# Kernel tuning notes

Measured on AMD Instinct MI355X. Metric: run time of the kernel, lower is better.

Reference implementation:

```python
import jax, jax.numpy as jnp
import numpy as np

DIM = 512
NUM_GROUPS = 32
NUM_HEADS = 8
EPS = 1e-5


def group_norm(x, gamma, beta):
    # x: (B, C, H, W); normalize over (C//G, H, W) per group
    B, C, H, W = x.shape
    g = x.reshape(B, NUM_GROUPS, -1)
    mean = g.mean(axis=2, keepdims=True)
    var = g.var(axis=2, keepdims=True)
    g = (g - mean) * jax.lax.rsqrt(var + EPS)
    x = g.reshape(B, C, H, W)
    return x * gamma[None, :, None, None] + beta[None, :, None, None]


def setup_inputs() -> dict:
    key = jax.random.key(0)
    ks = jax.random.split(key, 7)
    B, C, H, W = 16, DIM, 32, 32
    x = jax.random.normal(ks[0], (B, C, H, W), dtype=jnp.float32)
    gamma = jnp.ones((C,), dtype=jnp.float32)
    beta = jnp.zeros((C,), dtype=jnp.float32)
    s_in = 1.0 / np.sqrt(C)
    w_qkv = jax.random.normal(ks[1], (3 * C, C), dtype=jnp.float32) * s_in
    b_qkv = jnp.zeros((3 * C,), dtype=jnp.float32)
    w_proj = jax.random.normal(ks[2], (C, C), dtype=jnp.float32) * s_in
    b_proj = jnp.zeros((C,), dtype=jnp.float32)
    return {"x": x, "gamma": gamma, "beta": beta, "w_qkv": w_qkv,
            "b_qkv": b_qkv, "w_proj": w_proj, "b_proj": b_proj}


def reference(x, gamma, beta, w_qkv, b_qkv, w_proj, b_proj):
    B, C, H, W = x.shape
    nh = NUM_HEADS
    c3 = 3 * C // nh          # per-head qkv channels (3 * head_dim)
    dh = C // nh              # head_dim
    scale = C ** (-0.5)       # NOTE: source scales by full dim, not head_dim

    h = group_norm(x, gamma, beta)

    # 1x1 conv qkv projection: (B, 3C, H, W)
    qkv = jnp.einsum('bchw,oc->bohw', h, w_qkv) + b_qkv[None, :, None, None]

    # rearrange 'b (head c) h w -> (b head) (h w) c'
    qkv = qkv.reshape(B, nh, c3, H, W)
    qkv = qkv.transpose(0, 1, 3, 4, 2).reshape(B * nh, H * W, c3)
    q, k, v = jnp.split(qkv, 3, axis=2)   # each (B*nh, HW, dh)

    score = jnp.einsum('bnc,bmc->bnm', q, k * scale)   # (B*nh, HW, HW)
    attn = jax.nn.softmax(score, axis=2)
    out = jnp.einsum('bnm,bmc->bnc', attn, v)          # (B*nh, HW, dh)

    # rearrange '(head b) (h w) c -> b (head c) h w'  (NOTE head-major, as in source)
    out = out.reshape(nh, B, H, W, dh)
    out = out.transpose(1, 0, 4, 2, 3).reshape(B, C, H, W)

    out = jnp.einsum('bchw,oc->bohw', out, w_proj) + b_proj[None, :, None, None]
    return out + x
```

## Files before the change

kernel.cpp:

```cpp
#include <hip/hip_runtime.h>
#include <stdint.h>

typedef __bf16 bf16;
typedef __attribute__((ext_vector_type(4))) float f32x4;
typedef __attribute__((ext_vector_type(16))) float f32x16;
typedef __attribute__((ext_vector_type(4))) int i32x4;
typedef __attribute__((ext_vector_type(8))) __bf16 bf16x8;
typedef __attribute__((ext_vector_type(4))) __bf16 bf16x4;

#define NB 16
#define CH 512
#define HWS 1024
#define NHEAD 8
#define DH 64
#define O3 1536
#define CPQ 136
#define CPF 132
#define OPD 72

__device__ __forceinline__ void gload_lds16(const bf16* g, bf16* l) {
    __builtin_amdgcn_global_load_lds(
        (const __attribute__((address_space(1))) unsigned int*)g,
        (__attribute__((address_space(3))) unsigned int*)l,
        16, 0, 0);
}

#if defined(__has_builtin) && __has_builtin(__builtin_amdgcn_exp2f)
__device__ __forceinline__ float fast_exp2(float x) { return __builtin_amdgcn_exp2f(x); }
#else
__device__ __forceinline__ float fast_exp2(float x) { return exp2f(x); }
#endif

__device__ __forceinline__ unsigned int pkbf(float a, float b) {
    unsigned short lo = __builtin_bit_cast(unsigned short, (bf16)a);
    unsigned short hi = __builtin_bit_cast(unsigned short, (bf16)b);
    return (unsigned int)lo | ((unsigned int)hi << 16);
}

__global__ void prep(const float* __restrict__ x, float* __restrict__ stats,
                     const float* __restrict__ wq, const float* __restrict__ wp,
                     bf16* __restrict__ wq_b, bf16* __restrict__ wp_b) {
    int bx = blockIdx.x;
    if (bx < 512) {
        int b = bx >> 5, g = bx & 31;
        const float4* p = (const float4*)(x + ((size_t)(b * CH + g * 16)) * HWS);
        float s = 0.f, ss = 0.f;
        for (int i = threadIdx.x; i < 4096; i += 256) {
            float4 v = p[i];
            s  += v.x + v.y + v.z + v.w;
            ss += v.x*v.x + v.y*v.y + v.z*v.z + v.w*v.w;
        }
        for (int off = 32; off; off >>= 1) {
            s  += __shfl_xor(s,  off, 64);
            ss += __shfl_xor(ss, off, 64);
        }
        __shared__ float red[8];
        int w = threadIdx.x >> 6;
        if ((threadIdx.x & 63) == 0) { red[w*2] = s; red[w*2+1] = ss; }
        __syncthreads();
        if (threadIdx.x == 0) {
            float S  = red[0] + red[2] + red[4] + red[6];
            float SS = red[1] + red[3] + red[5] + red[7];
            float mean = S * (1.f/16384.f);
            float var  = SS * (1.f/16384.f) - mean*mean;
            stats[bx*2]   = mean;
            stats[bx*2+1] = rsqrtf(var + 1e-5f);
        }
    } else {
        int i = (bx - 512) * 256 + threadIdx.x;
        if (i < O3*CH) wq_b[i] = (bf16)wq[i];
        else           wp_b[i - O3*CH] = (bf16)wp[i - O3*CH];
    }
}

__global__ void gn_apply_t(const float* __restrict__ x, const float* __restrict__ stats,
                           const float* __restrict__ gamma, const float* __restrict__ beta,
                           bf16* __restrict__ hT) {
    __shared__ float tile[32][33];
    int bx = blockIdx.x;
    int b = bx >> 9;
    int rem = bx & 511;
    int ct = rem >> 5, nt = rem & 31;
    int tx = threadIdx.x & 31, ty = threadIdx.x >> 5;
    #pragma unroll
    for (int r = 0; r < 4; ++r) {
        int c = ct*32 + ty + r*8;
        int n = nt*32 + tx;
        float v = x[((size_t)(b * CH + c)) * HWS + n];
        int g = c >> 4;
        float mean = stats[(b*32+g)*2], rstd = stats[(b*32+g)*2+1];
        tile[ty + r*8][tx] = (v - mean) * rstd * gamma[c] + beta[c];
    }
    __syncthreads();
    #pragma unroll
    for (int r = 0; r < 4; ++r) {
        int n = nt*32 + ty + r*8;
        int c = ct*32 + tx;
        hT[((size_t)(b * HWS + n)) * CH + c] = (bf16)tile[tx][ty + r*8];
    }
}

__global__ __launch_bounds__(256, 3)
void qkv_gemm(const bf16* __restrict__ W, const bf16* __restrict__ hT,
              const float* __restrict__ bias, bf16* __restrict__ qkv,
              bf16* __restrict__ vT) {
    __shared__ __align__(16) bf16 SMEM[128*CPQ];
    bf16* As = SMEM;
    bf16* Bs = SMEM + 8192;
    int bx = blockIdx.x;
    int po = bx >> 7, qo = bx & 127;
    int obase = po*128, bnbase = qo*128;
    int tid = threadIdx.x;
    int lane = tid & 63, w = tid >> 6;
    int quad = lane >> 4, l15 = lane & 15;
    int wm = w >> 1, wn = w & 1;
    int x7 = l15 & 7;
    int srow = lane >> 3, spos = lane & 7;
    int sgc = (spos ^ srow) * 8;

    f32x4 acc[4][4] = {};
    for (int k0 = 0; k0 < 512; k0 += 64) {
        #pragma unroll
        for (int r = 0; r < 4; ++r) {
            int rb = r*32 + w*8;
            gload_lds16(W  + ((size_t)(obase  + rb + srow))*512 + k0 + sgc, &As[rb*64]);
            gload_lds16(hT + ((size_t)(bnbase + rb + srow))*512 + k0 + sgc, &Bs[rb*64]);
        }
        __syncthreads();
        #pragma unroll
        for (int ks = 0; ks < 2; ++ks) {
            int ch = (ks*4 + quad) ^ x7;
            bf16x8 af[4], bfv[4];
            #pragma unroll
            for (int mt = 0; mt < 4; ++mt)
                af[mt] = *(const bf16x8*)(&As[(wm*64 + mt*16 + l15)*64 + ch*8]);
            #pragma unroll
            for (int nt = 0; nt < 4; ++nt)
                bfv[nt] = *(const bf16x8*)(&Bs[(wn*64 + nt*16 + l15)*64 + ch*8]);
            #pragma unroll
            for (int mt = 0; mt < 4; ++mt)
                #pragma unroll
                for (int nt = 0; nt < 4; ++nt)
                    acc[mt][nt] = __builtin_amdgcn_mfma_f32_16x16x32_bf16(af[mt], bfv[nt], acc[mt][nt], 0, 0, 0);
        }
        __syncthreads();
    }

    bf16* Cs = SMEM;
    int b = bnbase >> 10;
    int nbase = bnbase & 1023;
    #pragma unroll
    for (int mt = 0; mt < 4; ++mt) {
        int o0 = obase + wm*64 + mt*16 + quad*4;
        float4 bb = *(const float4*)(bias + o0);
        int c192 = o0 % 192;
        bool isV = (c192 >= 128);
        int h = o0 / 192;
        int d0 = c192 - 128;
        #pragma unroll
        for (int nt = 0; nt < 4; ++nt) {
            int bn_l = wn*64 + nt*16 + l15;
            bf16x4 v;
            v[0] = (bf16)(acc[mt][nt][0] + bb.x);
            v[1] = (bf16)(acc[mt][nt][1] + bb.y);
            v[2] = (bf16)(acc[mt][nt][2] + bb.z);
            v[3] = (bf16)(acc[mt][nt][3] + bb.w);
            *(bf16x4*)(&Cs[bn_l*CPQ + (o0 - obase)]) = v;
            if (isV) {
                int key = nbase + bn_l;
                size_t vb_ = ((size_t)((b*8 + h)*64 + d0)) * HWS + key;
                vT[vb_]          = v[0];
                vT[vb_ + HWS]    = v[1];
                vT[vb_ + 2*HWS]  = v[2];
                vT[vb_ + 3*HWS]  = v[3];
            }
        }
    }
    __syncthreads();
    #pragma unroll
    for (int p = 0; p < 8; ++p) {
        int bn_l = p*16 + (tid >> 4);
        int o8 = (tid & 15) * 8;
        if ((obase + o8) % 192 < 128) {
            uint4 v = *(const uint4*)(&Cs[bn_l*CPQ + o8]);
            *(uint4*)(qkv + ((size_t)(bnbase + bn_l)) * O3 + obase + o8) = v;
        }
    }
}

__global__ __launch_bounds__(256, 3)
void flash_attn(const bf16* __restrict__ qkv, const bf16* __restrict__ vT,
                bf16* __restrict__ A2) {
    __shared__ __align__(16) bf16 Ks[2][64*64];
    __shared__ __align__(16) bf16 Vs[2][64*64];
    __shared__ __align__(16) bf16 Ps[4][32*OPD];
    int bx = blockIdx.x;
    int g = bx & 127, qt = bx >> 7;
    int b = g >> 3, h = g & 7;
    int tid = threadIdx.x, lane = tid & 63, w = tid >> 6;
    int l31 = lane & 31, hi = lane >> 5;
    bool hib = (hi != 0);
    int x7l = l31 & 7;
    int srow = lane >> 3, spos = lane & 7;
    int sgc = (spos ^ srow) * 8;
    const float kLog2 = 0.04419417382415922f * 1.44269504088896341f;

    bf16x8 aq[4];
    {
        int qrow = qt*128 + w*32 + l31;
        const bf16* qb = qkv + ((size_t)(b * HWS + qrow)) * O3 + h*192 + hi*8;
        #pragma unroll
        for (int seg = 0; seg < 4; ++seg) {
            aq[seg] = *(const bf16x8*)(qb + seg*16);
            #pragma unroll
            for (int j = 0; j < 8; ++j)
                aq[seg][j] = (bf16)((float)aq[seg][j] * kLog2);
        }
    }

    const bf16* kg = qkv + ((size_t)(b*HWS + w*16 + srow))*O3 + h*192 + 64 + sgc;
    const bf16* vg = vT  + ((size_t)(g*DH  + w*16 + srow))*HWS + sgc;

    gload_lds16(kg,                  &Ks[0][(w*16)*64]);
    gload_lds16(kg + (size_t)8*O3,   &Ks[0][(w*16 + 8)*64]);
    gload_lds16(vg,                  &Vs[0][(w*16)*64]);
    gload_lds16(vg + (size_t)8*HWS,  &Vs[0][(w*16 + 8)*64]);

    f32x16 acc[2] = {};
    f32x4 L4 = {};
    __syncthreads();

    for (int kt = 0; kt < 16; ++kt) {
        int cur = kt & 1;
        if (kt < 15) {
            gload_lds16(kg + (size_t)((kt+1)*64)*O3,     &Ks[cur^1][(w*16)*64]);
            gload_lds16(kg + (size_t)((kt+1)*64 + 8)*O3, &Ks[cur^1][(w*16 + 8)*64]);
            gload_lds16(vg + (kt+1)*64,                  &Vs[cur^1][(w*16)*64]);
            gload_lds16(vg + (size_t)8*HWS + (kt+1)*64,  &Vs[cur^1][(w*16 + 8)*64]);
        }
        const bf16* Kc = &Ks[cur][0];
        const bf16* Vc = &Vs[cur][0];

        bf16x8 pa[4];
        #pragma unroll
        for (int kb = 0; kb < 2; ++kb) {
            f32x16 z = {};
            #pragma unroll
            for (int seg = 0; seg < 4; ++seg) {
                bf16x8 ak = *(const bf16x8*)(&Kc[(kb*32 + l31)*64 + (((seg*2 + hi) ^ x7l)*8)]);
                z = __builtin_amdgcn_mfma_f32_32x32x16_bf16(ak, aq[seg], z, 0, 0, 0);
            }
            float e[16];
            #pragma unroll
            for (int r = 0; r < 16; ++r) {
                e[r] = fast_exp2(z[r]);
                L4[r & 3] += e[r];
            }
            unsigned int w8[8];
            #pragma unroll
            for (int i = 0; i < 8; ++i)
                w8[i] = pkbf(e[2*i], e[2*i + 1]);
            unsigned int p0 = __shfl_xor((int)w8[0], 32, 64);
            unsigned int p1 = __shfl_xor((int)w8[1], 32, 64);
            unsigned int p2 = __shfl_xor((int)w8[2], 32, 64);
            unsigned int p3 = __shfl_xor((int)w8[3], 32, 64);
            unsigned int p4 = __shfl_xor((int)w8[4], 32, 64);
            unsigned int p5 = __shfl_xor((int)w8[5], 32, 64);
            unsigned int p6 = __shfl_xor((int)w8[6], 32, 64);
            unsigned int p7 = __shfl_xor((int)w8[7], 32, 64);
            i32x4 f0, f1;
            f0[0] = (int)(hib ? p2 : w8[0]);
            f0[1] = (int)(hib ? p3 : w8[1]);
            f0[2] = (int)(hib ? w8[2] : p0);
            f0[3] = (int)(hib ? w8[3] : p1);
            f1[0] = (int)(hib ? p6 : w8[4]);
            f1[1] = (int)(hib ? p7 : w8[5]);
            f1[2] = (int)(hib ? w8[6] : p4);
            f1[3] = (int)(hib ? w8[7] : p5);
            pa[kb*2 + 0] = __builtin_bit_cast(bf16x8, f0);
            pa[kb*2 + 1] = __builtin_bit_cast(bf16x8, f1);
        }

        #pragma unroll
        for (int db = 0; db < 2; ++db)
            #pragma unroll
            for (int ks = 0; ks < 4; ++ks) {
                bf16x8 av = *(const bf16x8*)(&Vc[(db*32 + l31)*64 + (((ks*2 + hi) ^ x7l)*8)]);
                acc[db] = __builtin_amdgcn_mfma_f32_32x32x16_bf16(av, pa[ks], acc[db], 0, 0, 0);
            }
        __syncthreads();
    }

    float Lf = (L4[0] + L4[1]) + (L4[2] + L4[3]);
    Lf += __shfl_xor(Lf, 32, 64);
    float Linv = 1.f / Lf;

    bf16* Psw = &Ps[w][0];
    #pragma unroll
    for (int db = 0; db < 2; ++db)
        #pragma unroll
        for (int i = 0; i < 8; ++i) {
            int d = db*32 + (i >> 1)*8 + (i & 1)*2 + 4*hi;
            unsigned int wv = pkbf(acc[db][2*i] * Linv, acc[db][2*i + 1] * Linv);
            *(unsigned int*)(&Psw[l31*OPD + d]) = wv;
        }

    int bp = g & 15;
    int hp = g >> 4;
    #pragma unroll
    for (int cc = 0; cc < 4; ++cc) {
        int idx = cc*64 + lane;
        int q = idx >> 3, dcc = idx & 7;
        uint4 v = *(const uint4*)(&Psw[q*OPD + dcc*8]);
        size_t oidx = ((size_t)(bp * HWS + qt*128 + w*32 + q)) * CH + hp*64 + dcc*8;
        *(uint4*)(A2 + oidx) = v;
    }
}

__global__ __launch_bounds__(256, 3)
void proj_gemm(const bf16* __restrict__ A2, const bf16* __restrict__ Wp,
               const float* __restrict__ bias, const float* __restrict__ x,
               float* __restrict__ out) {
    __shared__ __align__(16) bf16 SMEM[16896];
    bf16* As = SMEM;
    bf16* Bs = SMEM + 8192;
    int bx = blockIdx.x;
    int po = bx >> 7, qo = bx & 127;
    int obase = po*128, bnbase = qo*128;
    int tid = threadIdx.x;
    int lane = tid & 63, w = tid >> 6;
    int quad = lane >> 4, l15 = lane & 15;
    int wm = w >> 1, wn = w & 1;
    int x7 = l15 & 7;
    int srow = lane >> 3, spos = lane & 7;
    int sgc = (spos ^ srow) * 8;

    f32x4 acc[4][4] = {};
    for (int k0 = 0; k0 < 512; k0 += 64) {
        #pragma unroll
        for (int r = 0; r < 4; ++r) {
            int rb = r*32 + w*8;
            gload_lds16(A2 + ((size_t)(bnbase + rb + srow))*512 + k0 + sgc, &As[rb*64]);
            gload_lds16(Wp + ((size_t)(obase  + rb + srow))*512 + k0 + sgc, &Bs[rb*64]);
        }
        __syncthreads();
        #pragma unroll
        for (int ks = 0; ks < 2; ++ks) {
            int ch = (ks*4 + quad) ^ x7;
            bf16x8 af[4], bfv[4];
            #pragma unroll
            for (int mt = 0; mt < 4; ++mt)
                af[mt] = *(const bf16x8*)(&As[(wm*64 + mt*16 + l15)*64 + ch*8]);
            #pragma unroll
            for (int nt = 0; nt < 4; ++nt)
                bfv[nt] = *(const bf16x8*)(&Bs[(wn*64 + nt*16 + l15)*64 + ch*8]);
            #pragma unroll
            for (int mt = 0; mt < 4; ++mt)
                #pragma unroll
                for (int nt = 0; nt < 4; ++nt)
                    acc[mt][nt] = __builtin_amdgcn_mfma_f32_16x16x32_bf16(af[mt], bfv[nt], acc[mt][nt], 0, 0, 0);
        }
        __syncthreads();
    }

    float* Cf = (float*)SMEM;
    int bb = bnbase >> 10;
    int nbase = bnbase & 1023;
    #pragma unroll
    for (int hh = 0; hh < 2; ++hh) {
        if (wm == hh) {
            #pragma unroll
            for (int mt = 0; mt < 4; ++mt)
                #pragma unroll
                for (int nt = 0; nt < 4; ++nt)
                    #pragma unroll
                    for (int r = 0; r < 4; ++r)
                        Cf[(mt*16 + quad*4 + r)*CPF + wn*64 + nt*16 + l15] = acc[mt][nt][r];
        }
        __syncthreads();
        #pragma unroll
        for (int p = 0; p < 4; ++p) {
            int ol = p*32 + (tid >> 3);
            int nl0 = (tid & 7) * 8;
            int o = obase + ol;
            float bv = bias[o];
            #pragma unroll
            for (int jj = 0; jj < 2; ++jj) {
                int nl = nl0 + jj*4;
                size_t idx = ((size_t)(bb * CH + o)) * HWS + nbase + hh*64 + nl;
                float4 xr = *(const float4*)(x + idx);
                float4 res;
                res.x = Cf[(nl+0)*CPF + ol] + bv + xr.x;
                res.y = Cf[(nl+1)*CPF + ol] + bv + xr.y;
                res.z = Cf[(nl+2)*CPF + ol] + bv + xr.z;
                res.w = Cf[(nl+3)*CPF + ol] + bv + xr.w;
                *(float4*)(out + idx) = res;
            }
        }
        __syncthreads();
    }
}

extern "C" void kernel_launch(void* const* d_in, const int* in_sizes, int n_in,
                              void* d_out, int out_size, void* d_ws, size_t ws_size,
                              hipStream_t stream) {
    const float* x      = (const float*)d_in[0];
    const float* gamma  = (const float*)d_in[1];
    const float* beta   = (const float*)d_in[2];
    const float* w_qkv  = (const float*)d_in[3];
    const float* b_qkv  = (const float*)d_in[4];
    const float* w_proj = (const float*)d_in[5];
    const float* b_proj = (const float*)d_in[6];
    float* out = (float*)d_out;

    char* ws = (char*)d_ws;
    float* stats = (float*)(ws + 0);
    bf16*  wq_b  = (bf16*)(ws + 4096);
    bf16*  wp_b  = (bf16*)(ws + 1576960);
    bf16*  hT    = (bf16*)(ws + 2101248);
    bf16*  qkv   = (bf16*)(ws + 18878464);
    bf16*  vT    = (bf16*)(ws + 69210112);
    bf16*  A2    = hT;

    prep       <<<4608, 256, 0, stream>>>(x, stats, w_qkv, w_proj, wq_b, wp_b);
    gn_apply_t <<<8192, 256, 0, stream>>>(x, stats, gamma, beta, hT);
    qkv_gemm   <<<1536, 256, 0, stream>>>(wq_b, hT, b_qkv, qkv, vT);
    flash_attn <<<1024, 256, 0, stream>>>(qkv, vT, A2);
    proj_gemm  <<<512,  256, 0, stream>>>(A2, wp_b, b_proj, x, out);
}
```

Before: 220.6 us.

## Widen flash attention blocks to 8 waves and use permlane32 swaps

The flash attention kernel now runs 512 threads per block, covering 256 query rows instead of 128, and the grid is halved. Each double-buffered K/V tile is shared by twice as many waves, which halves global K/V traffic per query, and each wave now issues one async LDS load per tensor per tile instead of two. The P-fragment exchange between half-waves now uses inline-asm v_permlane32_swap instead of eight cross-lane shuffles plus selects. The larger block and the tighter launch bound of 512 threads with 4 blocks may raise register pressure or cause spills, and there are fewer blocks to balance across compute units.

New measurement: 198.4 us. -10.1%, faster.

```diff
diff --git a/kernel.cpp b/kernel.cpp
--- a/kernel.cpp
+++ b/kernel.cpp
@@ -188,18 +188,17 @@
     }
 }
 
-__global__ __launch_bounds__(256, 3)
+__global__ __launch_bounds__(512, 4)
 void flash_attn(const bf16* __restrict__ qkv, const bf16* __restrict__ vT,
                 bf16* __restrict__ A2) {
     __shared__ __align__(16) bf16 Ks[2][64*64];
     __shared__ __align__(16) bf16 Vs[2][64*64];
-    __shared__ __align__(16) bf16 Ps[4][32*OPD];
+    __shared__ __align__(16) bf16 Ps[8][32*OPD];
     int bx = blockIdx.x;
     int g = bx & 127, qt = bx >> 7;
     int b = g >> 3, h = g & 7;
     int tid = threadIdx.x, lane = tid & 63, w = tid >> 6;
     int l31 = lane & 31, hi = lane >> 5;
-    bool hib = (hi != 0);
     int x7l = l31 & 7;
     int srow = lane >> 3, spos = lane & 7;
     int sgc = (spos ^ srow) * 8;
@@ -207,7 +206,7 @@
 
     bf16x8 aq[4];
     {
-        int qrow = qt*128 + w*32 + l31;
+        int qrow = qt*256 + w*32 + l31;
         const bf16* qb = qkv + ((size_t)(b * HWS + qrow)) * O3 + h*192 + hi*8;
         #pragma unroll
         for (int seg = 0; seg < 4; ++seg) {
@@ -218,13 +217,11 @@
         }
     }
 
-    const bf16* kg = qkv + ((size_t)(b*HWS + w*16 + srow))*O3 + h*192 + 64 + sgc;
-    const bf16* vg = vT  + ((size_t)(g*DH  + w*16 + srow))*HWS + sgc;
-
-    gload_lds16(kg,                  &Ks[0][(w*16)*64]);
-    gload_lds16(kg + (size_t)8*O3,   &Ks[0][(w*16 + 8)*64]);
-    gload_lds16(vg,                  &Vs[0][(w*16)*64]);
-    gload_lds16(vg + (size_t)8*HWS,  &Vs[0][(w*16 + 8)*64]);
+    const bf16* kg = qkv + ((size_t)(b*HWS + w*8 + srow))*O3 + h*192 + 64 + sgc;
+    const bf16* vg = vT  + ((size_t)(g*DH  + w*8 + srow))*HWS + sgc;
+
+    gload_lds16(kg, &Ks[0][w*512]);
+    gload_lds16(vg, &Vs[0][w*512]);
 
     f32x16 acc[2] = {};
     f32x4 L4 = {};
@@ -233,10 +230,8 @@
     for (int kt = 0; kt < 16; ++kt) {
         int cur = kt & 1;
         if (kt < 15) {
-            gload_lds16(kg + (size_t)((kt+1)*64)*O3,     &Ks[cur^1][(w*16)*64]);
-            gload_lds16(kg + (size_t)((kt+1)*64 + 8)*O3, &Ks[cur^1][(w*16 + 8)*64]);
-            gload_lds16(vg + (kt+1)*64,                  &Vs[cur^1][(w*16)*64]);
-            gload_lds16(vg + (size_t)8*HWS + (kt+1)*64,  &Vs[cur^1][(w*16 + 8)*64]);
+            gload_lds16(kg + (size_t)((kt+1)*64)*O3, &Ks[cur^1][w*512]);
+            gload_lds16(vg + (kt+1)*64,              &Vs[cur^1][w*512]);
         }
         const bf16* Kc = &Ks[cur][0];
         const bf16* Vc = &Vs[cur][0];
@@ -260,25 +255,16 @@
             #pragma unroll
             for (int i = 0; i < 8; ++i)
                 w8[i] = pkbf(e[2*i], e[2*i + 1]);
-            unsigned int p0 = __shfl_xor((int)w8[0], 32, 64);
-            unsigned int p1 = __shfl_xor((int)w8[1], 32, 64);
-            unsigned int p2 = __shfl_xor((int)w8[2], 32, 64);
-            unsigned int p3 = __shfl_xor((int)w8[3], 32, 64);
-            unsigned int p4 = __shfl_xor((int)w8[4], 32, 64);
-            unsigned int p5 = __shfl_xor((int)w8[5], 32, 64);
-            unsigned int p6 = __shfl_xor((int)w8[6], 32, 64);
-            unsigned int p7 = __shfl_xor((int)w8[7], 32, 64);
-            i32x4 f0, f1;
-            f0[0] = (int)(hib ? p2 : w8[0]);
-            f0[1] = (int)(hib ? p3 : w8[1]);
-            f0[2] = (int)(hib ? w8[2] : p0);
-            f0[3] = (int)(hib ? w8[3] : p1);
-            f1[0] = (int)(hib ? p6 : w8[4]);
-            f1[1] = (int)(hib ? p7 : w8[5]);
-            f1[2] = (int)(hib ? w8[6] : p4);
-            f1[3] = (int)(hib ? w8[7] : p5);
-            pa[kb*2 + 0] = __builtin_bit_cast(bf16x8, f0);
-            pa[kb*2 + 1] = __builtin_bit_cast(bf16x8, f1);
+            #pragma unroll
+            for (int kl = 0; kl < 2; ++kl) {
+                unsigned int a0 = w8[4*kl + 0], a1 = w8[4*kl + 1];
+                unsigned int b0 = w8[4*kl + 2], b1 = w8[4*kl + 3];
+                asm("v_permlane32_swap_b32 %0, %1" : "+v"(a0), "+v"(b0));
+                asm("v_permlane32_swap_b32 %0, %1" : "+v"(a1), "+v"(b1));
+                i32x4 f;
+                f[0] = (int)a0; f[1] = (int)a1; f[2] = (int)b0; f[3] = (int)b1;
+                pa[kb*2 + kl] = __builtin_bit_cast(bf16x8, f);
+            }
         }
 
         #pragma unroll
@@ -312,7 +298,7 @@
         int idx = cc*64 + lane;
         int q = idx >> 3, dcc = idx & 7;
         uint4 v = *(const uint4*)(&Psw[q*OPD + dcc*8]);
-        size_t oidx = ((size_t)(bp * HWS + qt*128 + w*32 + q)) * CH + hp*64 + dcc*8;
+        size_t oidx = ((size_t)(bp * HWS + qt*256 + w*32 + q)) * CH + hp*64 + dcc*8;
         *(uint4*)(A2 + oidx) = v;
     }
 }
@@ -425,6 +411,6 @@
     prep       <<<4608, 256, 0, stream>>>(x, stats, w_qkv, w_proj, wq_b, wp_b);
     gn_apply_t <<<8192, 256, 0, stream>>>(x, stats, gamma, beta, hT);
     qkv_gemm   <<<1536, 256, 0, stream>>>(wq_b, hT, b_qkv, qkv, vT);
-    flash_attn <<<1024, 256, 0, stream>>>(qkv, vT, A2);
+    flash_attn <<<512,  512, 0, stream>>>(qkv, vT, A2);
     proj_gemm  <<<512,  256, 0, stream>>>(A2, wp_b, b_proj, x, out);
 }
```
